# Kernel optimization log

Hardware: AMD Instinct MI355X
Metric: run time of the kernel (lower is better)

Reference implementation:

```python
import jax, jax.numpy as jnp
import numpy as np

PC_RANGE = np.array([-40.0, -40.0, -1.0, 40.0, 40.0, 5.4], np.float32)
RADIUS = 39.0
STEP_SIZE = 0.5
WORLD_LEN = 200
NUM_CLASSES = 17
FAST_THRES = 1e-7
W_ENT = 0.01
W_DIST = 0.01
W_SEM = 1.0
ALPHA_INIT = 1e-6

_xyz_min_w = PC_RANGE[:3]
_xyz_max_w = PC_RANGE[3:]
_rng = _xyz_max_w - _xyz_min_w
BG_LEN = float((np.floor_divide(_rng[0], 2.0) - RADIUS) / RADIUS)
SCENE_CENTER = ((_xyz_min_w + _xyz_max_w) * 0.5).astype(np.float32)
_Z = float(_rng[2] / _rng[0])
XYZ_MIN = np.array([-1.0 - BG_LEN, -1.0 - BG_LEN, -_Z], np.float32)
XYZ_MAX = np.array([1.0 + BG_LEN, 1.0 + BG_LEN, _Z], np.float32)
ACT_SHIFT = float(np.log(1.0 / (1.0 - ALPHA_INIT) - 1.0))
DIST_THRES = (2.0 + 2.0 * BG_LEN) / WORLD_LEN * STEP_SIZE * 0.95

N_INNER = int(2.0 / (2.0 + 2.0 * BG_LEN) * WORLD_LEN / STEP_SIZE) + 1
N_OUTER = N_INNER // 15
_b_in = np.linspace(0.0, 2.0, N_INNER + 1)
_b_out = 2.0 / np.linspace(1.0, 1.0 / 64.0, N_OUTER + 1)
T_VALS = np.concatenate([(_b_in[1:] + _b_in[:-1]) * 0.5, (_b_out[1:] + _b_out[:-1]) * 0.5]).astype(np.float32)

_freq = np.array([1163161, 2309034, 188743, 2997643, 20317180, 852476, 243808, 2457947, 497017, 2731022, 7224789, 214411435, 5565043, 63191967, 76098082, 128860031, 141625221], np.float64)
CLASS_W = (1.0 / np.log(_freq + 0.001)).astype(np.float32)


def trilinear(vol, g):
    # vol: [X,Y,Z,C]; g: [P,3] fractional voxel indices (align_corners=True, zeros padding)
    sizes = jnp.array(vol.shape[:3])
    g0f = jnp.floor(g)
    frac = g - g0f
    g0 = g0f.astype(jnp.int32)
    out = jnp.zeros((g.shape[0], vol.shape[3]), vol.dtype)
    for dx in (0, 1):
        for dy in (0, 1):
            for dz in (0, 1):
                off = jnp.array([dx, dy, dz])
                idx = g0 + off
                w = jnp.prod(jnp.where(off == 1, frac, 1.0 - frac), axis=-1)
                valid = jnp.all((idx >= 0) & (idx < sizes), axis=-1)
                ic = jnp.clip(idx, 0, sizes - 1)
                v = vol[ic[:, 0], ic[:, 1], ic[:, 2]]
                out = out + (w * valid)[:, None] * v
    return out


def _render_losses(density_b, semantic_b, rays_b, bda_b):
    t = jnp.asarray(T_VALS)  # [S]
    gt_depth = rays_b[:, 2]
    gt_depth = jnp.where(gt_depth > 52.0, 0.0, gt_depth)
    ray_valid = gt_depth > 0.0  # [N]
    gt_sem = rays_b[:, 3].astype(jnp.int32)
    ro = rays_b[:, 4:7]
    rd = rays_b[:, 7:10]
    rays_o = (ro - SCENE_CENTER) / RADIUS
    rays_d = rd / jnp.linalg.norm(rd, axis=-1, keepdims=True)
    pts = rays_o[:, None, :] + rays_d[:, None, :] * t[None, :, None]  # [N,S,3]
    nrm = jnp.linalg.norm(pts, axis=-1, keepdims=True)
    inner = (nrm <= 1.0)[..., 0]
    pts = jnp.where(nrm <= 1.0, pts, pts / nrm * (1.0 + BG_LEN - BG_LEN / nrm))
    pts = jnp.einsum('ij,nsj->nsi', bda_b, pts)
    # cumdist_thres: sequential cumulative-distance scan per ray (keep outer points spaced > thres)
    dist = jnp.linalg.norm(pts[:, 1:] - pts[:, :-1], axis=-1)  # [N,S-1]
    def step(cum, d):
        cum = cum + d
        over = cum > DIST_THRES
        return jnp.where(over, 0.0, cum), over
    _, over = jax.lax.scan(step, jnp.zeros(pts.shape[0], pts.dtype), dist.T)
    keep = jnp.concatenate([inner[:, :1], inner[:, 1:] | over.T], axis=1)
    # trilinear grid sample (align_corners=True)
    g = (pts - XYZ_MIN) / (XYZ_MAX - XYZ_MIN)
    gi = (g * (jnp.array([200.0, 200.0, 16.0]) - 1.0)).reshape(-1, 3)
    dens = trilinear(density_b[..., None], gi)[:, 0].reshape(pts.shape[:2])  # [N,S]
    sem = trilinear(semantic_b, gi).reshape(pts.shape[0], pts.shape[1], NUM_CLASSES)  # [N,S,C]
    # Raw2Alpha with interval=0.5: alpha = 1 - (1+exp(d+shift))^(-interval)
    alpha = 1.0 - jnp.power(1.0 + jnp.exp(dens + ACT_SHIFT), -0.5)
    alpha = jnp.where(keep & ray_valid[:, None], alpha, 0.0)
    alpha = jnp.where(alpha > FAST_THRES, alpha, 0.0)  # fast_color_thres cull
    # Alphas2Weights: per-ray exclusive transmittance cumprod
    om = 1.0 - alpha
    Tinc = jnp.cumprod(om, axis=1)
    Texcl = jnp.concatenate([jnp.ones_like(Tinc[:, :1]), Tinc[:, :-1]], axis=1)
    weights = alpha * Texcl
    alphainv_last = Tinc[:, -1]
    pk = weights > FAST_THRES
    w = jnp.where(pk, weights, 0.0)
    # segment_coo semantic render (segment-sum over step dim)
    sem_r = jnp.einsum('ns,nsc->nc', w, sem)
    logp = jax.nn.log_softmax(sem_r, axis=-1)
    nll = -jnp.take_along_axis(logp, gt_sem[:, None], axis=1)[:, 0]
    cw = jnp.asarray(CLASS_W)
    wy = cw[gt_sem] * ray_valid.astype(cw.dtype)
    loss_sem = jnp.sum(wy * nll) / jnp.maximum(jnp.sum(wy), 1e-12)
    # entropy of last transmittance over valid rays
    p = jnp.clip(alphainv_last, 1e-6, 1.0 - 1e-6)
    ent = -(p * jnp.log(p) + (1.0 - p) * jnp.log(1.0 - p))
    nv = jnp.maximum(jnp.sum(ray_valid), 1)
    loss_ent = jnp.sum(jnp.where(ray_valid, ent, 0.0)) / nv
    # flatten_eff_distloss with interval = 1/n_max
    s = 1.0 - 1.0 / (1.0 + t)
    m = jnp.broadcast_to(s[None, :], w.shape)
    n_max = jnp.maximum(jnp.sum(pk), 1)
    interval = 1.0 / n_max
    wm = w * m
    wp = jnp.cumsum(w, axis=1) - w
    wmp = jnp.cumsum(wm, axis=1) - wm
    loss_bi = 2.0 * w * (m * wp - wmp)
    loss_uni = (1.0 / 3.0) * interval * w * w
    loss_dist = (jnp.sum(loss_bi) + jnp.sum(loss_uni)) / nv
    return W_SEM * loss_sem, W_ENT * loss_ent, W_DIST * loss_dist


def setup_inputs():
    key = jax.random.key(0)
    ks = jax.random.split(key, 6)
    B, N = 1, 8192
    density = jax.random.normal(ks[0], (B, 200, 200, 16), jnp.float32)
    semantic = jax.random.normal(ks[1], (B, 200, 200, 16, 17), jnp.float32)
    depth = jax.random.uniform(ks[2], (B, N), jnp.float32, 0.1, 60.0)
    sem_lbl = jax.random.randint(ks[3], (B, N), 0, 17).astype(jnp.float32)
    ro = jax.random.normal(ks[4], (B, N, 3), jnp.float32) + jnp.array([0.0, 0.0, 1.5])
    rd = jax.random.normal(ks[5], (B, N, 3), jnp.float32)
    rd = rd / jnp.linalg.norm(rd, axis=-1, keepdims=True)
    rays = jnp.concatenate([jnp.zeros((B, N, 2)), depth[..., None], sem_lbl[..., None], ro, rd], axis=-1)
    bda = jnp.broadcast_to(jnp.eye(3, dtype=jnp.float32), (B, 3, 3))
    return {"density": density, "semantic": semantic, "rays": rays, "bda": bda}


def reference(density, semantic, rays, bda):
    B = density.shape[0]
    ls, le, ld = 0.0, 0.0, 0.0
    for b in range(B):
        a, c, d = _render_losses(density[b], semantic[b], rays[b], bda[b])
        ls, le, ld = ls + a, le + c, ld + d
    return (ls / B, le / B, ld / B)
```

## Files before the change

kernel.cpp:

```cpp
#include <hip/hip_runtime.h>
#include <math.h>


#define DXX 200
#define DYY 200
#define DZZ 16
#define NC 17
#define S_TOT 416
#define N_IN 390
#define CHUNKS 7
#define NBINS 8
#define BINSTRIDE 16
#define T_OFF 128

typedef float v4u __attribute__((ext_vector_type(4), aligned(4), may_alias));
typedef float v2u __attribute__((ext_vector_type(2), aligned(4), may_alias));
typedef float v4a __attribute__((ext_vector_type(4), aligned(16)));

__constant__ double c_freq[NC] = {1163161.0, 2309034.0, 188743.0, 2997643.0,
  20317180.0, 852476.0, 243808.0, 2457947.0, 497017.0, 2731022.0, 7224789.0,
  214411435.0, 5565043.0, 63191967.0, 76098082.0, 128860031.0, 141625221.0};

__device__ __forceinline__ float iscan_add(float x, int lane) {
#pragma unroll
  for (int off = 1; off < 64; off <<= 1) {
    float y = __shfl_up(x, off);
    if (lane >= off) x += y;
  }
  return x;
}
__device__ __forceinline__ float iscan_mul(float x, int lane) {
#pragma unroll
  for (int off = 1; off < 64; off <<= 1) {
    float y = __shfl_up(x, off);
    if (lane >= off) x *= y;
  }
  return x;
}

__global__ __launch_bounds__(512) void nerf_zero(float* acc) {
  int i = threadIdx.x;
  if (i < NBINS * BINSTRIDE) acc[i] = 0.f;
  if (i < CHUNKS * 64) {
    double td;
    if (i < N_IN) {
      td = (2.0 * i + 1.0) / 390.0;
    } else {
      int j = i - N_IN;
      const double stp = (1.0 / 64.0 - 1.0) / 26.0;
      double l0 = 1.0 + j * stp;
      double l1 = (j + 1 >= 26) ? (1.0 / 64.0) : (1.0 + (j + 1) * stp);
      td = 1.0 / l0 + 1.0 / l1;
    }
    acc[T_OFF + i] = (float)td;
  }
}

__global__ __launch_bounds__(256) void nerf_warm(
    const v4a* __restrict__ sem, int nsem4,
    const v4a* __restrict__ den, int nden4) {
  float s = 0.f;
  int stride = gridDim.x * blockDim.x;
  for (int i = blockIdx.x * blockDim.x + threadIdx.x; i < nsem4; i += stride) {
    v4a v = sem[i];
    s += v[0] + v[1] + v[2] + v[3];
  }
  for (int i = blockIdx.x * blockDim.x + threadIdx.x; i < nden4; i += stride) {
    v4a v = den[i];
    s += v[0] + v[1] + v[2] + v[3];
  }
  asm volatile("" :: "v"(s));
}

__global__ __launch_bounds__(64) void nerf_main(
    const float* __restrict__ density,
    const float* __restrict__ semantic,
    const float* __restrict__ rays,
    const float* __restrict__ bda,
    float* __restrict__ acc_g,
    int nrays) {
  __shared__ float s_t[CHUNKS * 64];
  __shared__ float s_dist[S_TOT];
  __shared__ unsigned long long s_keep[CHUNKS];
  __shared__ unsigned long long s_big[CHUNKS];

  const int lane = threadIdx.x;
  const int ray = blockIdx.x;
  if (ray >= nrays) return;

  const double BG = (double)(1.0f / 39.0f);
  const float BGf = (float)BG;
  const float DTH = (float)((2.0 + 2.0 * BG) / 200.0 * 0.5 * 0.95);
  const float xminf = (float)(-1.0 - BG);
  const float zf = 6.4f / 80.0f;
  const float sxy = 199.0f / ((float)(1.0 + BG) - xminf);
  const float szc = 15.0f / (zf + zf);
  const float ACTS = -13.815509557964274f;

  const float* rp = rays + (size_t)ray * 10;
  float dep = rp[2];
  if (!((dep > 0.f) && (dep <= 52.f))) return;
  int ysem = (int)rp[3];
  ysem = ysem < 0 ? 0 : (ysem > NC - 1 ? NC - 1 : ysem);
  const float czc = (-1.0f + 5.4f) * 0.5f;
  float rox = rp[4] / 39.0f;
  float roy = rp[5] / 39.0f;
  float roz = (rp[6] - czc) / 39.0f;
  float d0 = rp[7], d1 = rp[8], d2 = rp[9];
  float rn = sqrtf(d0 * d0 + d1 * d1 + d2 * d2);
  float rdx = d0 / rn, rdy = d1 / rn, rdz = d2 / rn;

  const float* g_t = acc_g + T_OFF;
#pragma unroll
  for (int i = 0; i < CHUNKS; i++) s_t[i * 64 + lane] = g_t[i * 64 + lane];
  asm volatile("s_waitcnt lgkmcnt(0)" ::: "memory");

  const float b00 = bda[0], b01 = bda[1], b02 = bda[2];
  const float b10 = bda[3], b11 = bda[4], b12 = bda[5];
  const float b20 = bda[6], b21 = bda[7], b22 = bda[8];

  auto compute_pt = [&](int s, float& tx, float& ty, float& tz, float& tt,
                        bool& inner) {
    tt = s_t[s];
    float qx = rox + rdx * tt;
    float qy = roy + rdy * tt;
    float qz = roz + rdz * tt;
    float nr = sqrtf(qx * qx + qy * qy + qz * qz);
    inner = (nr <= 1.0f) && (s < S_TOT);
    if (nr > 1.0f) {
      float sc = (1.0f + BGf - BGf / nr) / nr;
      qx *= sc; qy *= sc; qz *= sc;
    }
    tx = b00 * qx + b01 * qy + b02 * qz;
    ty = b10 * qx + b11 * qy + b12 * qz;
    tz = b20 * qx + b21 * qy + b22 * qz;
  };

  for (int c = 0; c < CHUNKS; c++) {
    int s = c * 64 + lane;
    float tx, ty, tz, tt; bool inner;
    compute_pt(s, tx, ty, tz, tt, inner);
    unsigned long long bal = __ballot(inner);
    float nx = __shfl(tx, lane + 1);
    float ny = __shfl(ty, lane + 1);
    float nz = __shfl(tz, lane + 1);
    if (c < CHUNKS - 1) {
      float hx, hy, hz, ht; bool hi;
      compute_pt((c + 1) * 64, hx, hy, hz, ht, hi);
      if (lane == 63) { nx = hx; ny = hy; nz = hz; }
    }
    float ex = nx - tx, ey = ny - ty, ez = nz - tz;
    float dd = sqrtf(ex * ex + ey * ey + ez * ez);
    bool dlive = (s < S_TOT - 1);
    if (dlive) s_dist[s] = dd;
    unsigned long long db = __ballot(dlive && (dd > DTH));
    if (lane == 0) { s_keep[c] = bal; s_big[c] = db; }
  }

  asm volatile("s_waitcnt lgkmcnt(0)" ::: "memory");
  if (lane == 0) {
    float cum = 0.f;
    int prev = 0;
    unsigned long long carrybit = 0;
#pragma unroll
    for (int c = 0; c < CHUNKS; c++) {
      unsigned long long inner = s_keep[c];
      unsigned long long db = s_big[c];
      unsigned long long big = (db << 1) | carrybit;
      carrybit = db >> 63;
      unsigned long long valid = ~0ull;
      if (c == 0) valid &= ~1ull;
      if (c == CHUNKS - 1) valid &= 0x00000000FFFFFFFFull;
      big &= valid;
      unsigned long long k = inner | big;
      unsigned long long nb = valid & ~big;
      while (nb) {
        int b = __ffsll((unsigned long long)nb) - 1;
        nb &= nb - 1;
        int s = c * 64 + b;
        if (s - 1 != prev) cum = 0.f;
        cum += s_dist[s - 1];
        if (cum > DTH) { cum = 0.f; k |= 1ull << b; }
        prev = s;
      }
      s_keep[c] = k;
    }
  }
  asm volatile("s_waitcnt lgkmcnt(0)" ::: "memory");

  float out_sem[NC];
#pragma unroll
  for (int j = 0; j < NC; j++) out_sem[j] = 0.f;
  float carry = 1.f, carryW = 0.f, carryWM = 0.f;
  float sum_bi = 0.f, sum_w2 = 0.f, pkcf = 0.f;

  for (int c = 0; c < CHUNKS; c++) {
    unsigned long long km = s_keep[c];
    if (km == 0ull) continue;
    int s = c * 64 + lane;
    float tx, ty, tz, tt; bool inner;
    compute_pt(s, tx, ty, tz, tt, inner);
    float m_ = 1.0f - 1.0f / (1.0f + tt);
    bool keep = (km >> lane) & 1ull;

    float gx = (tx - xminf) * sxy;
    float gy = (ty - xminf) * sxy;
    float gz = (tz + zf) * szc;
    float hxf = floorf(gx), hyf = floorf(gy), hzf = floorf(gz);
    int ix = (int)hxf, iy = (int)hyf, iz = (int)hzf;
    float fx = gx - hxf, fy = gy - hyf, fz = gz - hzf;
    float wx0 = 1.f - fx, wy0 = 1.f - fy, wz0 = 1.f - fz;
    bool vx0 = (unsigned)ix < (unsigned)DXX, vx1 = (unsigned)(ix + 1) < (unsigned)DXX;
    bool vy0 = (unsigned)iy < (unsigned)DYY, vy1 = (unsigned)(iy + 1) < (unsigned)DYY;
    bool vz0 = (unsigned)iz < (unsigned)DZZ, vz1 = (unsigned)(iz + 1) < (unsigned)DZZ;

    float a = 0.f;
    if (keep) {
      float dens = 0.f;
      const float* p0 = density + (ix * DYY + iy) * DZZ + iz;
      if (vx0 && vx1 && vy0 && vy1 && vz0 && vz1) {
        v2u d00 = *(const v2u*)(p0);
        v2u d01 = *(const v2u*)(p0 + DZZ);
        v2u d10 = *(const v2u*)(p0 + DYY * DZZ);
        v2u d11 = *(const v2u*)(p0 + DYY * DZZ + DZZ);
        dens += wx0 * wy0 * wz0 * d00[0];
        dens += wx0 * wy0 * fz  * d00[1];
        dens += wx0 * fy  * wz0 * d01[0];
        dens += wx0 * fy  * fz  * d01[1];
        dens += fx  * wy0 * wz0 * d10[0];
        dens += fx  * wy0 * fz  * d10[1];
        dens += fx  * fy  * wz0 * d11[0];
        dens += fx  * fy  * fz  * d11[1];
      } else {
        if (vx0 && vy0 && vz0) dens += wx0 * wy0 * wz0 * p0[0];
        if (vx0 && vy0 && vz1) dens += wx0 * wy0 * fz  * p0[1];
        if (vx0 && vy1 && vz0) dens += wx0 * fy  * wz0 * p0[DZZ];
        if (vx0 && vy1 && vz1) dens += wx0 * fy  * fz  * p0[DZZ + 1];
        if (vx1 && vy0 && vz0) dens += fx  * wy0 * wz0 * p0[DYY * DZZ];
        if (vx1 && vy0 && vz1) dens += fx  * wy0 * fz  * p0[DYY * DZZ + 1];
        if (vx1 && vy1 && vz0) dens += fx  * fy  * wz0 * p0[DYY * DZZ + DZZ];
        if (vx1 && vy1 && vz1) dens += fx  * fy  * fz  * p0[DYY * DZZ + DZZ + 1];
      }
      float u = expf(dens + ACTS);
      a = -expm1f(-0.5f * log1pf(u));
      if (!(a > 1e-7f)) a = 0.f;
    }

    float om = 1.f - a;
    float ip = iscan_mul(om, lane);
    float ex = __shfl_up(ip, 1); if (lane == 0) ex = 1.f;
    float wgt = a * carry * ex;
    carry *= __shfl(ip, 63);
    float w = (wgt > 1e-7f) ? wgt : 0.f;
    if (w > 0.f) pkcf += 1.f;

    float wm = w * m_;
    float isw = iscan_add(w, lane);
    float iswm = iscan_add(wm, lane);
    float exw = __shfl_up(isw, 1);  if (lane == 0) exw = 0.f;
    float exwm = __shfl_up(iswm, 1); if (lane == 0) exwm = 0.f;
    sum_bi += 2.f * w * (m_ * (carryW + exw) - (carryWM + exwm));
    sum_w2 += w * w;
    carryW += __shfl(isw, 63);
    carryWM += __shfl(iswm, 63);

    if (w > 0.f) {
      const float* sp0 = semantic + (size_t)((ix * DYY + iy) * DZZ + iz) * NC;
      const float* sp1 = sp0 + DYY * DZZ * NC;
#define SEM_ACC(PTR, WC)                                                        \
      { float wc = (WC);                                                        \
        const v4u* q = (const v4u*)(PTR);                                       \
        v4u q0 = q[0], q1 = q[1], q2 = q[2], q3 = q[3];                         \
        float qs = (PTR)[16];                                                   \
        out_sem[0]  += wc * q0[0];  out_sem[1]  += wc * q0[1];                  \
        out_sem[2]  += wc * q0[2];  out_sem[3]  += wc * q0[3];                  \
        out_sem[4]  += wc * q1[0];  out_sem[5]  += wc * q1[1];                  \
        out_sem[6]  += wc * q1[2];  out_sem[7]  += wc * q1[3];                  \
        out_sem[8]  += wc * q2[0];  out_sem[9]  += wc * q2[1];                  \
        out_sem[10] += wc * q2[2];  out_sem[11] += wc * q2[3];                  \
        out_sem[12] += wc * q3[0];  out_sem[13] += wc * q3[1];                  \
        out_sem[14] += wc * q3[2];  out_sem[15] += wc * q3[3];                  \
        out_sem[16] += wc * qs; }
      if (vx0 && vx1 && vy0 && vy1 && vz0 && vz1) {
        SEM_ACC(sp0,                 w * wx0 * wy0 * wz0)
        SEM_ACC(sp0 + NC,            w * wx0 * wy0 * fz)
        SEM_ACC(sp0 + DZZ * NC,      w * wx0 * fy  * wz0)
        SEM_ACC(sp0 + DZZ * NC + NC, w * wx0 * fy  * fz)
        SEM_ACC(sp1,                 w * fx  * wy0 * wz0)
        SEM_ACC(sp1 + NC,            w * fx  * wy0 * fz)
        SEM_ACC(sp1 + DZZ * NC,      w * fx  * fy  * wz0)
        SEM_ACC(sp1 + DZZ * NC + NC, w * fx  * fy  * fz)
      } else {
        if (vx0 && vy0 && vz0) SEM_ACC(sp0,                 w * wx0 * wy0 * wz0)
        if (vx0 && vy0 && vz1) SEM_ACC(sp0 + NC,            w * wx0 * wy0 * fz)
        if (vx0 && vy1 && vz0) SEM_ACC(sp0 + DZZ * NC,      w * wx0 * fy  * wz0)
        if (vx0 && vy1 && vz1) SEM_ACC(sp0 + DZZ * NC + NC, w * wx0 * fy  * fz)
        if (vx1 && vy0 && vz0) SEM_ACC(sp1,                 w * fx  * wy0 * wz0)
        if (vx1 && vy0 && vz1) SEM_ACC(sp1 + NC,            w * fx  * wy0 * fz)
        if (vx1 && vy1 && vz0) SEM_ACC(sp1 + DZZ * NC,      w * fx  * fy  * wz0)
        if (vx1 && vy1 && vz1) SEM_ACC(sp1 + DZZ * NC + NC, w * fx  * fy  * fz)
      }
#undef SEM_ACC
    }
  }

  float r0 = sum_bi, r1 = sum_w2, r2 = pkcf;
#pragma unroll
  for (int off = 32; off >= 1; off >>= 1) {
    r0 += __shfl_xor(r0, off);
    r1 += __shfl_xor(r1, off);
    r2 += __shfl_xor(r2, off);
#pragma unroll
    for (int j = 0; j < NC; j++) out_sem[j] += __shfl_xor(out_sem[j], off);
  }
  if (lane == 0) {
    float M = out_sem[0];
#pragma unroll
    for (int j = 1; j < NC; j++) M = fmaxf(M, out_sem[j]);
    float se = 0.f;
#pragma unroll
    for (int j = 0; j < NC; j++) se += expf(out_sem[j] - M);
    float lse = M + logf(se);
    float sy = 0.f;
#pragma unroll
    for (int j = 0; j < NC; j++) if (j == ysem) sy = out_sem[j];
    float nll = lse - sy;
    float cw = (float)(1.0 / log(c_freq[ysem] + 0.001));
    float p = fminf(fmaxf(carry, 1e-6f), 1.0f - 1e-6f);
    float ent = -(p * logf(p) + (1.f - p) * logf(1.f - p));
    float* bin = acc_g + (ray & (NBINS - 1)) * BINSTRIDE;
    atomicAdd(&bin[0], cw * nll);
    atomicAdd(&bin[1], cw);
    atomicAdd(&bin[2], ent);
    atomicAdd(&bin[3], 1.f);
    atomicAdd(&bin[4], r0);
    atomicAdd(&bin[5], r1);
    atomicAdd(&bin[6], r2);
  }
}

__global__ __launch_bounds__(64) void nerf_fin(const float* __restrict__ acc,
                                               float* __restrict__ out) {
  if (threadIdx.x == 0) {
    float t0 = 0.f, t1 = 0.f, t2 = 0.f, t3 = 0.f, t4 = 0.f, t5 = 0.f, t6 = 0.f;
#pragma unroll
    for (int b = 0; b < NBINS; b++) {
      const float* p = acc + b * BINSTRIDE;
      t0 += p[0]; t1 += p[1]; t2 += p[2]; t3 += p[3];
      t4 += p[4]; t5 += p[5]; t6 += p[6];
    }
    float ls = t0 / fmaxf(t1, 1e-12f);
    float nv = fmaxf(t3, 1.f);
    float le = t2 / nv;
    float nmax = fmaxf(t6, 1.f);
    float ld = (t4 + (1.f / 3.f) * (1.f / nmax) * t5) / nv;
    out[0] = 1.0f * ls;
    out[1] = 0.01f * le;
    out[2] = 0.01f * ld;
  }
}

extern "C" void kernel_launch(void* const* d_in, const int* in_sizes, int n_in,
                              void* d_out, int out_size, void* d_ws, size_t ws_size,
                              hipStream_t stream) {
  const float* density = (const float*)d_in[0];
  const float* semantic = (const float*)d_in[1];
  const float* rays = (const float*)d_in[2];
  const float* bda = (const float*)d_in[3];
  float* out = (float*)d_out;
  float* acc = (float*)d_ws;
  int nrays = in_sizes[2] / 10;
  int nsem4 = (DXX * DYY * DZZ * NC) / 4;
  int nden4 = (DXX * DYY * DZZ) / 4;
  nerf_zero<<<1, 512, 0, stream>>>(acc);
  nerf_warm<<<2048, 256, 0, stream>>>((const v4a*)semantic, nsem4,
                                      (const v4a*)density, nden4);
  nerf_main<<<nrays, 64, 0, stream>>>(density, semantic, rays, bda, acc, nrays);
  nerf_fin<<<1, 64, 0, stream>>>(acc, out);
}
```

Measured before the change: 332.1 us.

## Drop cache-warm kernel, fuse finalize via last-block counter, pair z-neighbour semantic loads

```diff
diff --git a/kernel.cpp b/kernel.cpp
--- a/kernel.cpp
+++ b/kernel.cpp
@@ -12,10 +12,10 @@
 #define NBINS 8
 #define BINSTRIDE 16
 #define T_OFF 128
+#define CNT_OFF 1024
 
 typedef float v4u __attribute__((ext_vector_type(4), aligned(4), may_alias));
 typedef float v2u __attribute__((ext_vector_type(2), aligned(4), may_alias));
-typedef float v4a __attribute__((ext_vector_type(4), aligned(16)));
 
 __constant__ double c_freq[NC] = {1163161.0, 2309034.0, 188743.0, 2997643.0,
   20317180.0, 852476.0, 243808.0, 2457947.0, 497017.0, 2731022.0, 7224789.0,
@@ -41,6 +41,7 @@
 __global__ __launch_bounds__(512) void nerf_zero(float* acc) {
   int i = threadIdx.x;
   if (i < NBINS * BINSTRIDE) acc[i] = 0.f;
+  if (i == 0) ((int*)acc)[CNT_OFF] = 0;
   if (i < CHUNKS * 64) {
     double td;
     if (i < N_IN) {
@@ -56,28 +57,13 @@
   }
 }
 
-__global__ __launch_bounds__(256) void nerf_warm(
-    const v4a* __restrict__ sem, int nsem4,
-    const v4a* __restrict__ den, int nden4) {
-  float s = 0.f;
-  int stride = gridDim.x * blockDim.x;
-  for (int i = blockIdx.x * blockDim.x + threadIdx.x; i < nsem4; i += stride) {
-    v4a v = sem[i];
-    s += v[0] + v[1] + v[2] + v[3];
-  }
-  for (int i = blockIdx.x * blockDim.x + threadIdx.x; i < nden4; i += stride) {
-    v4a v = den[i];
-    s += v[0] + v[1] + v[2] + v[3];
-  }
-  asm volatile("" :: "v"(s));
-}
-
 __global__ __launch_bounds__(64) void nerf_main(
     const float* __restrict__ density,
     const float* __restrict__ semantic,
     const float* __restrict__ rays,
     const float* __restrict__ bda,
     float* __restrict__ acc_g,
+    float* __restrict__ out,
     int nrays) {
   __shared__ float s_t[CHUNKS * 64];
   __shared__ float s_dist[S_TOT];
@@ -86,7 +72,6 @@
 
   const int lane = threadIdx.x;
   const int ray = blockIdx.x;
-  if (ray >= nrays) return;
 
   const double BG = (double)(1.0f / 39.0f);
   const float BGf = (float)BG;
@@ -99,264 +84,299 @@
 
   const float* rp = rays + (size_t)ray * 10;
   float dep = rp[2];
-  if (!((dep > 0.f) && (dep <= 52.f))) return;
-  int ysem = (int)rp[3];
-  ysem = ysem < 0 ? 0 : (ysem > NC - 1 ? NC - 1 : ysem);
-  const float czc = (-1.0f + 5.4f) * 0.5f;
-  float rox = rp[4] / 39.0f;
-  float roy = rp[5] / 39.0f;
-  float roz = (rp[6] - czc) / 39.0f;
-  float d0 = rp[7], d1 = rp[8], d2 = rp[9];
-  float rn = sqrtf(d0 * d0 + d1 * d1 + d2 * d2);
-  float rdx = d0 / rn, rdy = d1 / rn, rdz = d2 / rn;
-
-  const float* g_t = acc_g + T_OFF;
-#pragma unroll
-  for (int i = 0; i < CHUNKS; i++) s_t[i * 64 + lane] = g_t[i * 64 + lane];
-  asm volatile("s_waitcnt lgkmcnt(0)" ::: "memory");
-
-  const float b00 = bda[0], b01 = bda[1], b02 = bda[2];
-  const float b10 = bda[3], b11 = bda[4], b12 = bda[5];
-  const float b20 = bda[6], b21 = bda[7], b22 = bda[8];
-
-  auto compute_pt = [&](int s, float& tx, float& ty, float& tz, float& tt,
-                        bool& inner) {
-    tt = s_t[s];
-    float qx = rox + rdx * tt;
-    float qy = roy + rdy * tt;
-    float qz = roz + rdz * tt;
-    float nr = sqrtf(qx * qx + qy * qy + qz * qz);
-    inner = (nr <= 1.0f) && (s < S_TOT);
-    if (nr > 1.0f) {
-      float sc = (1.0f + BGf - BGf / nr) / nr;
-      qx *= sc; qy *= sc; qz *= sc;
-    }
-    tx = b00 * qx + b01 * qy + b02 * qz;
-    ty = b10 * qx + b11 * qy + b12 * qz;
-    tz = b20 * qx + b21 * qy + b22 * qz;
-  };
-
-  for (int c = 0; c < CHUNKS; c++) {
-    int s = c * 64 + lane;
-    float tx, ty, tz, tt; bool inner;
-    compute_pt(s, tx, ty, tz, tt, inner);
-    unsigned long long bal = __ballot(inner);
-    float nx = __shfl(tx, lane + 1);
-    float ny = __shfl(ty, lane + 1);
-    float nz = __shfl(tz, lane + 1);
-    if (c < CHUNKS - 1) {
-      float hx, hy, hz, ht; bool hi;
-      compute_pt((c + 1) * 64, hx, hy, hz, ht, hi);
-      if (lane == 63) { nx = hx; ny = hy; nz = hz; }
-    }
-    float ex = nx - tx, ey = ny - ty, ez = nz - tz;
-    float dd = sqrtf(ex * ex + ey * ey + ez * ez);
-    bool dlive = (s < S_TOT - 1);
-    if (dlive) s_dist[s] = dd;
-    unsigned long long db = __ballot(dlive && (dd > DTH));
-    if (lane == 0) { s_keep[c] = bal; s_big[c] = db; }
-  }
-
-  asm volatile("s_waitcnt lgkmcnt(0)" ::: "memory");
+  bool valid = (ray < nrays) && (dep > 0.f) && (dep <= 52.f);
+
+  if (valid) {
+    int ysem = (int)rp[3];
+    ysem = ysem < 0 ? 0 : (ysem > NC - 1 ? NC - 1 : ysem);
+    const float czc = (-1.0f + 5.4f) * 0.5f;
+    float rox = rp[4] / 39.0f;
+    float roy = rp[5] / 39.0f;
+    float roz = (rp[6] - czc) / 39.0f;
+    float d0 = rp[7], d1 = rp[8], d2 = rp[9];
+    float rn = sqrtf(d0 * d0 + d1 * d1 + d2 * d2);
+    float rdx = d0 / rn, rdy = d1 / rn, rdz = d2 / rn;
+
+    const float* g_t = acc_g + T_OFF;
+#pragma unroll
+    for (int i = 0; i < CHUNKS; i++) s_t[i * 64 + lane] = g_t[i * 64 + lane];
+    asm volatile("s_waitcnt lgkmcnt(0)" ::: "memory");
+
+    const float b00 = bda[0], b01 = bda[1], b02 = bda[2];
+    const float b10 = bda[3], b11 = bda[4], b12 = bda[5];
+    const float b20 = bda[6], b21 = bda[7], b22 = bda[8];
+
+    auto compute_pt = [&](int s, float& tx, float& ty, float& tz, float& tt,
+                          bool& inner) {
+      tt = s_t[s];
+      float qx = rox + rdx * tt;
+      float qy = roy + rdy * tt;
+      float qz = roz + rdz * tt;
+      float nr = sqrtf(qx * qx + qy * qy + qz * qz);
+      inner = (nr <= 1.0f) && (s < S_TOT);
+      if (nr > 1.0f) {
+        float sc = (1.0f + BGf - BGf / nr) / nr;
+        qx *= sc; qy *= sc; qz *= sc;
+      }
+      tx = b00 * qx + b01 * qy + b02 * qz;
+      ty = b10 * qx + b11 * qy + b12 * qz;
+      tz = b20 * qx + b21 * qy + b22 * qz;
+    };
+
+    for (int c = 0; c < CHUNKS; c++) {
+      int s = c * 64 + lane;
+      float tx, ty, tz, tt; bool inner;
+      compute_pt(s, tx, ty, tz, tt, inner);
+      unsigned long long bal = __ballot(inner);
+      float nx = __shfl(tx, lane + 1);
+      float ny = __shfl(ty, lane + 1);
+      float nz = __shfl(tz, lane + 1);
+      if (c < CHUNKS - 1) {
+        float hx, hy, hz, ht; bool hi;
+        compute_pt((c + 1) * 64, hx, hy, hz, ht, hi);
+        if (lane == 63) { nx = hx; ny = hy; nz = hz; }
+      }
+      float ex = nx - tx, ey = ny - ty, ez = nz - tz;
+      float dd = sqrtf(ex * ex + ey * ey + ez * ez);
+      bool dlive = (s < S_TOT - 1);
+      if (dlive) s_dist[s] = dd;
+      unsigned long long db = __ballot(dlive && (dd > DTH));
+      if (lane == 0) { s_keep[c] = bal; s_big[c] = db; }
+    }
+
+    asm volatile("s_waitcnt lgkmcnt(0)" ::: "memory");
+    if (lane == 0) {
+      float cum = 0.f;
+      int prev = 0;
+      unsigned long long carrybit = 0;
+#pragma unroll
+      for (int c = 0; c < CHUNKS; c++) {
+        unsigned long long inner = s_keep[c];
+        unsigned long long db = s_big[c];
+        unsigned long long big = (db << 1) | carrybit;
+        carrybit = db >> 63;
+        unsigned long long vmask = ~0ull;
+        if (c == 0) vmask &= ~1ull;
+        if (c == CHUNKS - 1) vmask &= 0x00000000FFFFFFFFull;
+        big &= vmask;
+        unsigned long long k = inner | big;
+        unsigned long long nb = vmask & ~big;
+        while (nb) {
+          int b = __ffsll((unsigned long long)nb) - 1;
+          nb &= nb - 1;
+          int s = c * 64 + b;
+          if (s - 1 != prev) cum = 0.f;
+          cum += s_dist[s - 1];
+          if (cum > DTH) { cum = 0.f; k |= 1ull << b; }
+          prev = s;
+        }
+        s_keep[c] = k;
+      }
+    }
+    asm volatile("s_waitcnt lgkmcnt(0)" ::: "memory");
+
+    float out_sem[NC];
+#pragma unroll
+    for (int j = 0; j < NC; j++) out_sem[j] = 0.f;
+    float carry = 1.f, carryW = 0.f, carryWM = 0.f;
+    float sum_bi = 0.f, sum_w2 = 0.f, pkcf = 0.f;
+
+    for (int c = 0; c < CHUNKS; c++) {
+      unsigned long long km = s_keep[c];
+      if (km == 0ull) continue;
+      int s = c * 64 + lane;
+      float tx, ty, tz, tt; bool inner;
+      compute_pt(s, tx, ty, tz, tt, inner);
+      float m_ = 1.0f - 1.0f / (1.0f + tt);
+      bool keep = (km >> lane) & 1ull;
+
+      float gx = (tx - xminf) * sxy;
+      float gy = (ty - xminf) * sxy;
+      float gz = (tz + zf) * szc;
+      float hxf = floorf(gx), hyf = floorf(gy), hzf = floorf(gz);
+      int ix = (int)hxf, iy = (int)hyf, iz = (int)hzf;
+      float fx = gx - hxf, fy = gy - hyf, fz = gz - hzf;
+      float wx0 = 1.f - fx, wy0 = 1.f - fy, wz0 = 1.f - fz;
+      bool vx0 = (unsigned)ix < (unsigned)DXX, vx1 = (unsigned)(ix + 1) < (unsigned)DXX;
+      bool vy0 = (unsigned)iy < (unsigned)DYY, vy1 = (unsigned)(iy + 1) < (unsigned)DYY;
+      bool vz0 = (unsigned)iz < (unsigned)DZZ, vz1 = (unsigned)(iz + 1) < (unsigned)DZZ;
+
+      float a = 0.f;
+      if (keep) {
+        float dens = 0.f;
+        const float* p0 = density + (ix * DYY + iy) * DZZ + iz;
+        if (vx0 && vx1 && vy0 && vy1 && vz0 && vz1) {
+          v2u d00 = *(const v2u*)(p0);
+          v2u d01 = *(const v2u*)(p0 + DZZ);
+          v2u d10 = *(const v2u*)(p0 + DYY * DZZ);
+          v2u d11 = *(const v2u*)(p0 + DYY * DZZ + DZZ);
+          dens += wx0 * wy0 * wz0 * d00[0];
+          dens += wx0 * wy0 * fz  * d00[1];
+          dens += wx0 * fy  * wz0 * d01[0];
+          dens += wx0 * fy  * fz  * d01[1];
+          dens += fx  * wy0 * wz0 * d10[0];
+          dens += fx  * wy0 * fz  * d10[1];
+          dens += fx  * fy  * wz0 * d11[0];
+          dens += fx  * fy  * fz  * d11[1];
+        } else {
+          if (vx0 && vy0 && vz0) dens += wx0 * wy0 * wz0 * p0[0];
+          if (vx0 && vy0 && vz1) dens += wx0 * wy0 * fz  * p0[1];
+          if (vx0 && vy1 && vz0) dens += wx0 * fy  * wz0 * p0[DZZ];
+          if (vx0 && vy1 && vz1) dens += wx0 * fy  * fz  * p0[DZZ + 1];
+          if (vx1 && vy0 && vz0) dens += fx  * wy0 * wz0 * p0[DYY * DZZ];
+          if (vx1 && vy0 && vz1) dens += fx  * wy0 * fz  * p0[DYY * DZZ + 1];
+          if (vx1 && vy1 && vz0) dens += fx  * fy  * wz0 * p0[DYY * DZZ + DZZ];
+          if (vx1 && vy1 && vz1) dens += fx  * fy  * fz  * p0[DYY * DZZ + DZZ + 1];
+        }
+        float u = expf(dens + ACTS);
+        a = -expm1f(-0.5f * log1pf(u));
+        if (!(a > 1e-7f)) a = 0.f;
+      }
+
+      float om = 1.f - a;
+      float ip = iscan_mul(om, lane);
+      float ex = __shfl_up(ip, 1); if (lane == 0) ex = 1.f;
+      float wgt = a * carry * ex;
+      carry *= __shfl(ip, 63);
+      float w = (wgt > 1e-7f) ? wgt : 0.f;
+      if (w > 0.f) pkcf += 1.f;
+
+      if (w > 0.f) {
+        const float* spx0 = semantic + (size_t)((ix * DYY + iy) * DZZ + iz) * NC;
+        const float* spx1 = spx0 + DYY * DZZ * NC;
+#define SEM_ROW(PTR, WC)                                                        \
+        { float wc = (WC);                                                      \
+          const v4u* q = (const v4u*)(PTR);                                     \
+          v4u q0 = q[0], q1 = q[1], q2 = q[2], q3 = q[3];                       \
+          float qs = (PTR)[16];                                                 \
+          out_sem[0]  += wc * q0[0];  out_sem[1]  += wc * q0[1];                \
+          out_sem[2]  += wc * q0[2];  out_sem[3]  += wc * q0[3];                \
+          out_sem[4]  += wc * q1[0];  out_sem[5]  += wc * q1[1];                \
+          out_sem[6]  += wc * q1[2];  out_sem[7]  += wc * q1[3];                \
+          out_sem[8]  += wc * q2[0];  out_sem[9]  += wc * q2[1];                \
+          out_sem[10] += wc * q2[2];  out_sem[11] += wc * q2[3];                \
+          out_sem[12] += wc * q3[0];  out_sem[13] += wc * q3[1];                \
+          out_sem[14] += wc * q3[2];  out_sem[15] += wc * q3[3];                \
+          out_sem[16] += wc * qs; }
+#define SEM_SPAN(PTR, WC0, WC1)                                                 \
+        { float wca = (WC0), wcb = (WC1);                                       \
+          const v4u* q = (const v4u*)(PTR);                                     \
+          v4u q0 = q[0], q1 = q[1], q2 = q[2], q3 = q[3];                       \
+          v4u q4 = q[4], q5 = q[5], q6 = q[6], q7 = q[7];                       \
+          v2u qt = *(const v2u*)((PTR) + 32);                                   \
+          out_sem[0]  += wca * q0[0];  out_sem[1]  += wca * q0[1];              \
+          out_sem[2]  += wca * q0[2];  out_sem[3]  += wca * q0[3];              \
+          out_sem[4]  += wca * q1[0];  out_sem[5]  += wca * q1[1];              \
+          out_sem[6]  += wca * q1[2];  out_sem[7]  += wca * q1[3];              \
+          out_sem[8]  += wca * q2[0];  out_sem[9]  += wca * q2[1];              \
+          out_sem[10] += wca * q2[2];  out_sem[11] += wca * q2[3];              \
+          out_sem[12] += wca * q3[0];  out_sem[13] += wca * q3[1];              \
+          out_sem[14] += wca * q3[2];  out_sem[15] += wca * q3[3];              \
+          out_sem[16] += wca * q4[0];                                           \
+          out_sem[0]  += wcb * q4[1];  out_sem[1]  += wcb * q4[2];              \
+          out_sem[2]  += wcb * q4[3];  out_sem[3]  += wcb * q5[0];              \
+          out_sem[4]  += wcb * q5[1];  out_sem[5]  += wcb * q5[2];              \
+          out_sem[6]  += wcb * q5[3];  out_sem[7]  += wcb * q6[0];              \
+          out_sem[8]  += wcb * q6[1];  out_sem[9]  += wcb * q6[2];              \
+          out_sem[10] += wcb * q6[3];  out_sem[11] += wcb * q7[0];              \
+          out_sem[12] += wcb * q7[1];  out_sem[13] += wcb * q7[2];              \
+          out_sem[14] += wcb * q7[3];  out_sem[15] += wcb * qt[0];              \
+          out_sem[16] += wcb * qt[1]; }
+        bool zpair = vz0 && vz1;
+        if (vx0 && vy0) {
+          if (zpair)      SEM_SPAN(spx0, w * wx0 * wy0 * wz0, w * wx0 * wy0 * fz)
+          else if (vz0)   SEM_ROW(spx0,      w * wx0 * wy0 * wz0)
+          else if (vz1)   SEM_ROW(spx0 + NC, w * wx0 * wy0 * fz)
+        }
+        if (vx0 && vy1) {
+          const float* p = spx0 + DZZ * NC;
+          if (zpair)      SEM_SPAN(p, w * wx0 * fy * wz0, w * wx0 * fy * fz)
+          else if (vz0)   SEM_ROW(p,      w * wx0 * fy * wz0)
+          else if (vz1)   SEM_ROW(p + NC, w * wx0 * fy * fz)
+        }
+        if (vx1 && vy0) {
+          if (zpair)      SEM_SPAN(spx1, w * fx * wy0 * wz0, w * fx * wy0 * fz)
+          else if (vz0)   SEM_ROW(spx1,      w * fx * wy0 * wz0)
+          else if (vz1)   SEM_ROW(spx1 + NC, w * fx * wy0 * fz)
+        }
+        if (vx1 && vy1) {
+          const float* p = spx1 + DZZ * NC;
+          if (zpair)      SEM_SPAN(p, w * fx * fy * wz0, w * fx * fy * fz)
+          else if (vz0)   SEM_ROW(p,      w * fx * fy * wz0)
+          else if (vz1)   SEM_ROW(p + NC, w * fx * fy * fz)
+        }
+#undef SEM_ROW
+#undef SEM_SPAN
+      }
+
+      float wm = w * m_;
+      float isw = iscan_add(w, lane);
+      float iswm = iscan_add(wm, lane);
+      float exw = __shfl_up(isw, 1);  if (lane == 0) exw = 0.f;
+      float exwm = __shfl_up(iswm, 1); if (lane == 0) exwm = 0.f;
+      sum_bi += 2.f * w * (m_ * (carryW + exw) - (carryWM + exwm));
+      sum_w2 += w * w;
+      carryW += __shfl(isw, 63);
+      carryWM += __shfl(iswm, 63);
+    }
+
+    float r0 = sum_bi, r1 = sum_w2, r2 = pkcf;
+#pragma unroll
+    for (int off = 32; off >= 1; off >>= 1) {
+      r0 += __shfl_xor(r0, off);
+      r1 += __shfl_xor(r1, off);
+      r2 += __shfl_xor(r2, off);
+#pragma unroll
+      for (int j = 0; j < NC; j++) out_sem[j] += __shfl_xor(out_sem[j], off);
+    }
+    if (lane == 0) {
+      float M = out_sem[0];
+#pragma unroll
+      for (int j = 1; j < NC; j++) M = fmaxf(M, out_sem[j]);
+      float se = 0.f;
+#pragma unroll
+      for (int j = 0; j < NC; j++) se += expf(out_sem[j] - M);
+      float lse = M + logf(se);
+      float sy = 0.f;
+#pragma unroll
+      for (int j = 0; j < NC; j++) if (j == ysem) sy = out_sem[j];
+      float nll = lse - sy;
+      float cw = (float)(1.0 / log(c_freq[ysem] + 0.001));
+      float p = fminf(fmaxf(carry, 1e-6f), 1.0f - 1e-6f);
+      float ent = -(p * logf(p) + (1.f - p) * logf(1.f - p));
+      float* bin = acc_g + (ray & (NBINS - 1)) * BINSTRIDE;
+      atomicAdd(&bin[0], cw * nll);
+      atomicAdd(&bin[1], cw);
+      atomicAdd(&bin[2], ent);
+      atomicAdd(&bin[3], 1.f);
+      atomicAdd(&bin[4], r0);
+      atomicAdd(&bin[5], r1);
+      atomicAdd(&bin[6], r2);
+    }
+  }
+
   if (lane == 0) {
-    float cum = 0.f;
-    int prev = 0;
-    unsigned long long carrybit = 0;
-#pragma unroll
-    for (int c = 0; c < CHUNKS; c++) {
-      unsigned long long inner = s_keep[c];
-      unsigned long long db = s_big[c];
-      unsigned long long big = (db << 1) | carrybit;
-      carrybit = db >> 63;
-      unsigned long long valid = ~0ull;
-      if (c == 0) valid &= ~1ull;
-      if (c == CHUNKS - 1) valid &= 0x00000000FFFFFFFFull;
-      big &= valid;
-      unsigned long long k = inner | big;
-      unsigned long long nb = valid & ~big;
-      while (nb) {
-        int b = __ffsll((unsigned long long)nb) - 1;
-        nb &= nb - 1;
-        int s = c * 64 + b;
-        if (s - 1 != prev) cum = 0.f;
-        cum += s_dist[s - 1];
-        if (cum > DTH) { cum = 0.f; k |= 1ull << b; }
-        prev = s;
-      }
-      s_keep[c] = k;
-    }
-  }
-  asm volatile("s_waitcnt lgkmcnt(0)" ::: "memory");
-
-  float out_sem[NC];
-#pragma unroll
-  for (int j = 0; j < NC; j++) out_sem[j] = 0.f;
-  float carry = 1.f, carryW = 0.f, carryWM = 0.f;
-  float sum_bi = 0.f, sum_w2 = 0.f, pkcf = 0.f;
-
-  for (int c = 0; c < CHUNKS; c++) {
-    unsigned long long km = s_keep[c];
-    if (km == 0ull) continue;
-    int s = c * 64 + lane;
-    float tx, ty, tz, tt; bool inner;
-    compute_pt(s, tx, ty, tz, tt, inner);
-    float m_ = 1.0f - 1.0f / (1.0f + tt);
-    bool keep = (km >> lane) & 1ull;
-
-    float gx = (tx - xminf) * sxy;
-    float gy = (ty - xminf) * sxy;
-    float gz = (tz + zf) * szc;
-    float hxf = floorf(gx), hyf = floorf(gy), hzf = floorf(gz);
-    int ix = (int)hxf, iy = (int)hyf, iz = (int)hzf;
-    float fx = gx - hxf, fy = gy - hyf, fz = gz - hzf;
-    float wx0 = 1.f - fx, wy0 = 1.f - fy, wz0 = 1.f - fz;
-    bool vx0 = (unsigned)ix < (unsigned)DXX, vx1 = (unsigned)(ix + 1) < (unsigned)DXX;
-    bool vy0 = (unsigned)iy < (unsigned)DYY, vy1 = (unsigned)(iy + 1) < (unsigned)DYY;
-    bool vz0 = (unsigned)iz < (unsigned)DZZ, vz1 = (unsigned)(iz + 1) < (unsigned)DZZ;
-
-    float a = 0.f;
-    if (keep) {
-      float dens = 0.f;
-      const float* p0 = density + (ix * DYY + iy) * DZZ + iz;
-      if (vx0 && vx1 && vy0 && vy1 && vz0 && vz1) {
-        v2u d00 = *(const v2u*)(p0);
-        v2u d01 = *(const v2u*)(p0 + DZZ);
-        v2u d10 = *(const v2u*)(p0 + DYY * DZZ);
-        v2u d11 = *(const v2u*)(p0 + DYY * DZZ + DZZ);
-        dens += wx0 * wy0 * wz0 * d00[0];
-        dens += wx0 * wy0 * fz  * d00[1];
-        dens += wx0 * fy  * wz0 * d01[0];
-        dens += wx0 * fy  * fz  * d01[1];
-        dens += fx  * wy0 * wz0 * d10[0];
-        dens += fx  * wy0 * fz  * d10[1];
-        dens += fx  * fy  * wz0 * d11[0];
-        dens += fx  * fy  * fz  * d11[1];
-      } else {
-        if (vx0 && vy0 && vz0) dens += wx0 * wy0 * wz0 * p0[0];
-        if (vx0 && vy0 && vz1) dens += wx0 * wy0 * fz  * p0[1];
-        if (vx0 && vy1 && vz0) dens += wx0 * fy  * wz0 * p0[DZZ];
-        if (vx0 && vy1 && vz1) dens += wx0 * fy  * fz  * p0[DZZ + 1];
-        if (vx1 && vy0 && vz0) dens += fx  * wy0 * wz0 * p0[DYY * DZZ];
-        if (vx1 && vy0 && vz1) dens += fx  * wy0 * fz  * p0[DYY * DZZ + 1];
-        if (vx1 && vy1 && vz0) dens += fx  * fy  * wz0 * p0[DYY * DZZ + DZZ];
-        if (vx1 && vy1 && vz1) dens += fx  * fy  * fz  * p0[DYY * DZZ + DZZ + 1];
-      }
-      float u = expf(dens + ACTS);
-      a = -expm1f(-0.5f * log1pf(u));
-      if (!(a > 1e-7f)) a = 0.f;
-    }
-
-    float om = 1.f - a;
-    float ip = iscan_mul(om, lane);
-    float ex = __shfl_up(ip, 1); if (lane == 0) ex = 1.f;
-    float wgt = a * carry * ex;
-    carry *= __shfl(ip, 63);
-    float w = (wgt > 1e-7f) ? wgt : 0.f;
-    if (w > 0.f) pkcf += 1.f;
-
-    float wm = w * m_;
-    float isw = iscan_add(w, lane);
-    float iswm = iscan_add(wm, lane);
-    float exw = __shfl_up(isw, 1);  if (lane == 0) exw = 0.f;
-    float exwm = __shfl_up(iswm, 1); if (lane == 0) exwm = 0.f;
-    sum_bi += 2.f * w * (m_ * (carryW + exw) - (carryWM + exwm));
-    sum_w2 += w * w;
-    carryW += __shfl(isw, 63);
-    carryWM += __shfl(iswm, 63);
-
-    if (w > 0.f) {
-      const float* sp0 = semantic + (size_t)((ix * DYY + iy) * DZZ + iz) * NC;
-      const float* sp1 = sp0 + DYY * DZZ * NC;
-#define SEM_ACC(PTR, WC)                                                        \
-      { float wc = (WC);                                                        \
-        const v4u* q = (const v4u*)(PTR);                                       \
-        v4u q0 = q[0], q1 = q[1], q2 = q[2], q3 = q[3];                         \
-        float qs = (PTR)[16];                                                   \
-        out_sem[0]  += wc * q0[0];  out_sem[1]  += wc * q0[1];                  \
-        out_sem[2]  += wc * q0[2];  out_sem[3]  += wc * q0[3];                  \
-        out_sem[4]  += wc * q1[0];  out_sem[5]  += wc * q1[1];                  \
-        out_sem[6]  += wc * q1[2];  out_sem[7]  += wc * q1[3];                  \
-        out_sem[8]  += wc * q2[0];  out_sem[9]  += wc * q2[1];                  \
-        out_sem[10] += wc * q2[2];  out_sem[11] += wc * q2[3];                  \
-        out_sem[12] += wc * q3[0];  out_sem[13] += wc * q3[1];                  \
-        out_sem[14] += wc * q3[2];  out_sem[15] += wc * q3[3];                  \
-        out_sem[16] += wc * qs; }
-      if (vx0 && vx1 && vy0 && vy1 && vz0 && vz1) {
-        SEM_ACC(sp0,                 w * wx0 * wy0 * wz0)
-        SEM_ACC(sp0 + NC,            w * wx0 * wy0 * fz)
-        SEM_ACC(sp0 + DZZ * NC,      w * wx0 * fy  * wz0)
-        SEM_ACC(sp0 + DZZ * NC + NC, w * wx0 * fy  * fz)
-        SEM_ACC(sp1,                 w * fx  * wy0 * wz0)
-        SEM_ACC(sp1 + NC,            w * fx  * wy0 * fz)
-        SEM_ACC(sp1 + DZZ * NC,      w * fx  * fy  * wz0)
-        SEM_ACC(sp1 + DZZ * NC + NC, w * fx  * fy  * fz)
-      } else {
-        if (vx0 && vy0 && vz0) SEM_ACC(sp0,                 w * wx0 * wy0 * wz0)
-        if (vx0 && vy0 && vz1) SEM_ACC(sp0 + NC,            w * wx0 * wy0 * fz)
-        if (vx0 && vy1 && vz0) SEM_ACC(sp0 + DZZ * NC,      w * wx0 * fy  * wz0)
-        if (vx0 && vy1 && vz1) SEM_ACC(sp0 + DZZ * NC + NC, w * wx0 * fy  * fz)
-        if (vx1 && vy0 && vz0) SEM_ACC(sp1,                 w * fx  * wy0 * wz0)
-        if (vx1 && vy0 && vz1) SEM_ACC(sp1 + NC,            w * fx  * wy0 * fz)
-        if (vx1 && vy1 && vz0) SEM_ACC(sp1 + DZZ * NC,      w * fx  * fy  * wz0)
-        if (vx1 && vy1 && vz1) SEM_ACC(sp1 + DZZ * NC + NC, w * fx  * fy  * fz)
-      }
-#undef SEM_ACC
-    }
-  }
-
-  float r0 = sum_bi, r1 = sum_w2, r2 = pkcf;
-#pragma unroll
-  for (int off = 32; off >= 1; off >>= 1) {
-    r0 += __shfl_xor(r0, off);
-    r1 += __shfl_xor(r1, off);
-    r2 += __shfl_xor(r2, off);
-#pragma unroll
-    for (int j = 0; j < NC; j++) out_sem[j] += __shfl_xor(out_sem[j], off);
-  }
-  if (lane == 0) {
-    float M = out_sem[0];
-#pragma unroll
-    for (int j = 1; j < NC; j++) M = fmaxf(M, out_sem[j]);
-    float se = 0.f;
-#pragma unroll
-    for (int j = 0; j < NC; j++) se += expf(out_sem[j] - M);
-    float lse = M + logf(se);
-    float sy = 0.f;
-#pragma unroll
-    for (int j = 0; j < NC; j++) if (j == ysem) sy = out_sem[j];
-    float nll = lse - sy;
-    float cw = (float)(1.0 / log(c_freq[ysem] + 0.001));
-    float p = fminf(fmaxf(carry, 1e-6f), 1.0f - 1e-6f);
-    float ent = -(p * logf(p) + (1.f - p) * logf(1.f - p));
-    float* bin = acc_g + (ray & (NBINS - 1)) * BINSTRIDE;
-    atomicAdd(&bin[0], cw * nll);
-    atomicAdd(&bin[1], cw);
-    atomicAdd(&bin[2], ent);
-    atomicAdd(&bin[3], 1.f);
-    atomicAdd(&bin[4], r0);
-    atomicAdd(&bin[5], r1);
-    atomicAdd(&bin[6], r2);
-  }
-}
-
-__global__ __launch_bounds__(64) void nerf_fin(const float* __restrict__ acc,
-                                               float* __restrict__ out) {
-  if (threadIdx.x == 0) {
-    float t0 = 0.f, t1 = 0.f, t2 = 0.f, t3 = 0.f, t4 = 0.f, t5 = 0.f, t6 = 0.f;
-#pragma unroll
-    for (int b = 0; b < NBINS; b++) {
-      const float* p = acc + b * BINSTRIDE;
-      t0 += p[0]; t1 += p[1]; t2 += p[2]; t3 += p[3];
-      t4 += p[4]; t5 += p[5]; t6 += p[6];
-    }
-    float ls = t0 / fmaxf(t1, 1e-12f);
-    float nv = fmaxf(t3, 1.f);
-    float le = t2 / nv;
-    float nmax = fmaxf(t6, 1.f);
-    float ld = (t4 + (1.f / 3.f) * (1.f / nmax) * t5) / nv;
-    out[0] = 1.0f * ls;
-    out[1] = 0.01f * le;
-    out[2] = 0.01f * ld;
+    __threadfence();
+    int prev = atomicAdd((int*)acc_g + CNT_OFF, 1);
+    if (prev == (int)gridDim.x - 1) {
+      float t[7];
+#pragma unroll
+      for (int j = 0; j < 7; j++) t[j] = 0.f;
+#pragma unroll
+      for (int b = 0; b < NBINS; b++) {
+        float* p = acc_g + b * BINSTRIDE;
+#pragma unroll
+        for (int j = 0; j < 7; j++) t[j] += atomicAdd(&p[j], 0.f);
+      }
+      float ls = t[0] / fmaxf(t[1], 1e-12f);
+      float nv = fmaxf(t[3], 1.f);
+      float le = t[2] / nv;
+      float nmax = fmaxf(t[6], 1.f);
+      float ld = (t[4] + (1.f / 3.f) * (1.f / nmax) * t[5]) / nv;
+      out[0] = 1.0f * ls;
+      out[1] = 0.01f * le;
+      out[2] = 0.01f * ld;
+    }
   }
 }
 
@@ -370,11 +390,7 @@
   float* out = (float*)d_out;
   float* acc = (float*)d_ws;
   int nrays = in_sizes[2] / 10;
-  int nsem4 = (DXX * DYY * DZZ * NC) / 4;
-  int nden4 = (DXX * DYY * DZZ) / 4;
   nerf_zero<<<1, 512, 0, stream>>>(acc);
-  nerf_warm<<<2048, 256, 0, stream>>>((const v4a*)semantic, nsem4,
-                                      (const v4a*)density, nden4);
-  nerf_main<<<nrays, 64, 0, stream>>>(density, semantic, rays, bda, acc, nrays);
-  nerf_fin<<<1, 64, 0, stream>>>(acc, out);
-}
+  nerf_main<<<nrays, 64, 0, stream>>>(density, semantic, rays, bda, acc, out,
+                                      nrays);
+}
```

New measurement: 365.7 us. +10.1%, slower.
